# Kernel optimization log

Measured on AMD Instinct MI355X. Metric: run time of the kernel, lower is better.

## Reference

```python
import jax, jax.numpy as jnp
import numpy as np

SCALE = 100.0  # sharp-softmax temperature from the torch module

def _build_tables():
    # ByteToNibbleFFN: W1 is identity(256) so it is mathematically a no-op; keep W2.
    W2_b2n = np.zeros((256, 32), np.float32)
    bb = np.arange(256)
    W2_b2n[bb, bb >> 4] = 1.0
    W2_b2n[bb, 16 + (bb & 15)] = 1.0
    # NibbleAddWithCarryFFN tables
    W1_add = np.zeros((34, 512), np.float32)
    W2_sum = np.zeros((512, 16), np.float32)
    W2_cout = np.zeros((512, 2), np.float32)
    for a in range(16):
        for b in range(16):
            for c in range(2):
                idx = a * 32 + b * 2 + c
                W1_add[a, idx] = 1.0
                W1_add[16 + b, idx] = 1.0
                W1_add[32 + c, idx] = 1.0
                t = a + b + c
                W2_sum[idx, t & 15] = 1.0
                W2_cout[idx, 1 if t > 15 else 0] = 1.0
    # NibbleToByteFFN tables
    W1_n2b = np.zeros((32, 256), np.float32)
    W2_n2b = np.zeros((256, 256), np.float32)
    for h in range(16):
        for l in range(16):
            addr = h * 16 + l
            W1_n2b[h, addr] = 1.0
            W1_n2b[16 + l, addr] = 1.0
            W2_n2b[addr, (h << 4) | l] = 1.0
    return tuple(jnp.asarray(t) for t in (W2_b2n, W1_add, W2_sum, W2_cout, W1_n2b, W2_n2b))

W2_B2N, W1_ADD, W2_SUM, W2_COUT, W1_N2B, W2_N2B = _build_tables()

def _b2n(x):
    # byte [.,256] -> (high [.,16], low [.,16]); W1=eye(256) omitted (identity)
    out = x @ W2_B2N
    return out[..., :16], out[..., 16:]

def _nib_add(a, b, cin):
    combined = jnp.concatenate([a, b, cin], axis=-1)           # [.,34]
    address = jax.nn.softmax(combined @ W1_ADD * SCALE, axis=-1)  # [.,512]
    return address @ W2_SUM, address @ W2_COUT

def _n2b(high, low):
    combined = jnp.concatenate([high, low], axis=-1)           # [.,32]
    address = jax.nn.softmax(combined @ W1_N2B * SCALE, axis=-1)  # [.,256]
    return address @ W2_N2B

def setup_inputs() -> dict:
    key = jax.random.key(0)
    k1, k2 = jax.random.split(key)
    B = 32768
    a = jax.random.uniform(k1, (B, 4, 256), dtype=jnp.float32)
    b = jax.random.uniform(k2, (B, 4, 256), dtype=jnp.float32)
    return {"a": a, "b": b}

def reference(a, b):
    # NeuralALU.add: ripple-carry add over 4 bytes, 2 nibble adds per byte
    B = a.shape[0]
    carry = jnp.zeros((B, 2), a.dtype).at[:, 0].set(1.0)  # carry_zero one-hot
    out_bytes = []
    for i in range(4):  # fixed structural loop over bytes (carry dependence)
        ah, al = _b2n(a[:, i])
        bh, bl = _b2n(b[:, i])
        sl, carry = _nib_add(al, bl, carry)
        sh, carry = _nib_add(ah, bh, carry)
        out_bytes.append(_n2b(sh, sl))
    return jnp.stack(out_bytes, axis=1)  # [B,4,256]
```

## Files before the change

kernel.cpp:

```cpp
#include <hip/hip_runtime.h>

#define NIB_SCALE 100.0f
#define NWAVES_TOTAL 8192

template<int CTRL>
__device__ __forceinline__ float fdpp(float x) {
    return __int_as_float(__builtin_amdgcn_update_dpp(
        0, __float_as_int(x), CTRL, 0xF, 0xF, true));
}
__device__ __forceinline__ float fswz_xor4(float x) {
    return __int_as_float(__builtin_amdgcn_ds_swizzle(__float_as_int(x), 0x101F));
}
__device__ __forceinline__ float fbperm(int byteIdx, float v) {
    return __int_as_float(__builtin_amdgcn_ds_bpermute(byteIdx, __float_as_int(v)));
}

__device__ __forceinline__ float rsum16d(float v) {
    v += fdpp<0x121>(v); v += fdpp<0x122>(v); v += fdpp<0x124>(v); v += fdpp<0x128>(v);
    return v;
}
__device__ __forceinline__ float rmax16d(float v) {
    v = fmaxf(v, fdpp<0x121>(v)); v = fmaxf(v, fdpp<0x122>(v));
    v = fmaxf(v, fdpp<0x124>(v)); v = fmaxf(v, fdpp<0x128>(v));
    return v;
}
__device__ __forceinline__ float scan16d(float v) {
    v += fdpp<0x111>(v); v += fdpp<0x112>(v); v += fdpp<0x114>(v); v += fdpp<0x118>(v);
    return v;
}
__device__ __forceinline__ float softmax16d(float v) {
    float m = rmax16d(v);
    float e = __expf(NIB_SCALE * (v - m));
    float s = rsum16d(e);
    return e / s;
}
__device__ __forceinline__ float sharp_sigmoid(float c) {
    return 1.0f / (1.0f + __expf(NIB_SCALE * (1.0f - 2.0f * c)));
}

#define GATHER_ROT(dst, src)            \
    dst[0]  = (src);                    \
    dst[1]  = fdpp<0x121>(src);         \
    dst[2]  = fdpp<0x122>(src);         \
    dst[3]  = fdpp<0x123>(src);         \
    dst[4]  = fdpp<0x124>(src);         \
    dst[5]  = fdpp<0x125>(src);         \
    dst[6]  = fdpp<0x126>(src);         \
    dst[7]  = fdpp<0x127>(src);         \
    dst[8]  = fdpp<0x128>(src);         \
    dst[9]  = fdpp<0x129>(src);         \
    dst[10] = fdpp<0x12A>(src);         \
    dst[11] = fdpp<0x12B>(src);         \
    dst[12] = fdpp<0x12C>(src);         \
    dst[13] = fdpp<0x12D>(src);         \
    dst[14] = fdpp<0x12E>(src);         \
    dst[15] = fdpp<0x12F>(src);

__global__ __launch_bounds__(256, 6) void nalu_kernel(const float* __restrict__ A,
                                                      const float* __restrict__ B,
                                                      float* __restrict__ O,
                                                      int nrows) {
    __shared__ __align__(16) float sQL[16][16];
    __shared__ __align__(16) float sQH[16][16];
    __shared__ __align__(16) float sPSL[16][16];
    __shared__ __align__(16) float sPSH[16][16];
    __shared__ __align__(16) float sOV[4][4][4];

    const int tid = threadIdx.x;
    const int k = tid & 15;
    const int g = tid >> 4;
    const int b = g & 3;
    const int w = tid >> 6;
    const int lane64 = tid & 63;
    const int bpermIdx = 4 * ((lane64 & 48) | ((k & 3) << 2) | (k >> 2));
    const int wg = blockIdx.x * 4 + w;
    const int RP = (nrows + NWAVES_TOTAL - 1) / NWAVES_TOTAL;

    int row = wg;
    float4 cA0, cA1, cA2, cA3, cB0, cB1, cB2, cB3;
    if (row < nrows) {
        const float4* pa4 = (const float4*)(A + (long)row * 1024 + b * 256);
        const float4* pb4 = (const float4*)(B + (long)row * 1024 + b * 256);
        cA0 = pa4[k]; cA1 = pa4[16 + k]; cA2 = pa4[32 + k]; cA3 = pa4[48 + k];
        cB0 = pb4[k]; cB1 = pb4[16 + k]; cB2 = pb4[32 + k]; cB3 = pb4[48 + k];
    }

    for (int it = 0; it < RP; ++it) {
        const int nxtRow = row + NWAVES_TOTAL;

        float ahj[4], bhj[4];
        {
            float s;
            s = (cA0.x + cA0.y) + (cA0.z + cA0.w); s += fdpp<0xB1>(s); s += fdpp<0x4E>(s); ahj[0] = s;
            s = (cA1.x + cA1.y) + (cA1.z + cA1.w); s += fdpp<0xB1>(s); s += fdpp<0x4E>(s); ahj[1] = s;
            s = (cA2.x + cA2.y) + (cA2.z + cA2.w); s += fdpp<0xB1>(s); s += fdpp<0x4E>(s); ahj[2] = s;
            s = (cA3.x + cA3.y) + (cA3.z + cA3.w); s += fdpp<0xB1>(s); s += fdpp<0x4E>(s); ahj[3] = s;
            s = (cB0.x + cB0.y) + (cB0.z + cB0.w); s += fdpp<0xB1>(s); s += fdpp<0x4E>(s); bhj[0] = s;
            s = (cB1.x + cB1.y) + (cB1.z + cB1.w); s += fdpp<0xB1>(s); s += fdpp<0x4E>(s); bhj[1] = s;
            s = (cB2.x + cB2.y) + (cB2.z + cB2.w); s += fdpp<0xB1>(s); s += fdpp<0x4E>(s); bhj[2] = s;
            s = (cB3.x + cB3.y) + (cB3.z + cB3.w); s += fdpp<0xB1>(s); s += fdpp<0x4E>(s); bhj[3] = s;
        }
        float ali[4], bli[4];
        {
            float s;
            s = (cA0.x + cA1.x) + (cA2.x + cA3.x); s += fswz_xor4(s); s += fdpp<0x128>(s); ali[0] = s;
            s = (cA0.y + cA1.y) + (cA2.y + cA3.y); s += fswz_xor4(s); s += fdpp<0x128>(s); ali[1] = s;
            s = (cA0.z + cA1.z) + (cA2.z + cA3.z); s += fswz_xor4(s); s += fdpp<0x128>(s); ali[2] = s;
            s = (cA0.w + cA1.w) + (cA2.w + cA3.w); s += fswz_xor4(s); s += fdpp<0x128>(s); ali[3] = s;
            s = (cB0.x + cB1.x) + (cB2.x + cB3.x); s += fswz_xor4(s); s += fdpp<0x128>(s); bli[0] = s;
            s = (cB0.y + cB1.y) + (cB2.y + cB3.y); s += fswz_xor4(s); s += fdpp<0x128>(s); bli[1] = s;
            s = (cB0.z + cB1.z) + (cB2.z + cB3.z); s += fswz_xor4(s); s += fdpp<0x128>(s); bli[2] = s;
            s = (cB0.w + cB1.w) + (cB2.w + cB3.w); s += fswz_xor4(s); s += fdpp<0x128>(s); bli[3] = s;
        }
        float t0, t1;
        t0 = (k & 4) ? ali[1] : ali[0]; t1 = (k & 4) ? ali[3] : ali[2];
        float al = fbperm(bpermIdx, (k & 8) ? t1 : t0);
        t0 = (k & 4) ? bli[1] : bli[0]; t1 = (k & 4) ? bli[3] : bli[2];
        float bl = fbperm(bpermIdx, (k & 8) ? t1 : t0);
        t0 = (k & 1) ? ahj[1] : ahj[0]; t1 = (k & 1) ? ahj[3] : ahj[2];
        float ah = fbperm(bpermIdx, (k & 2) ? t1 : t0);
        t0 = (k & 1) ? bhj[1] : bhj[0]; t1 = (k & 1) ? bhj[3] : bhj[2];
        float bh = fbperm(bpermIdx, (k & 2) ? t1 : t0);

        const bool vn = (it + 1 < RP) && (nxtRow < nrows);
        if (vn) {
            const float4* pa4 = (const float4*)(A + (long)nxtRow * 1024 + b * 256);
            const float4* pb4 = (const float4*)(B + (long)nxtRow * 1024 + b * 256);
            cA0 = pa4[k]; cA1 = pa4[16 + k]; cA2 = pa4[32 + k]; cA3 = pa4[48 + k];
            cB0 = pb4[k]; cB1 = pb4[16 + k]; cB2 = pb4[32 + k]; cB3 = pb4[48 + k];
        }

        float pal = softmax16d(al);
        float pbl = softmax16d(bl);
        float pah = softmax16d(ah);
        float pbh = softmax16d(bh);

        sQL[g][k] = pbl;
        sQH[g][k] = pbh;

        float mirl = fdpp<0x140>(pbl);
        float mirh = fdpp<0x140>(pbh);
        float T15l = scan16d(mirl);
        float T15h = scan16d(mirh);
        float ov15l = rsum16d(pal * T15l);
        float c15l  = rsum16d(pal * mirl);
        float ov15h = rsum16d(pah * T15h);
        float c15h  = rsum16d(pah * mirh);
        float ov16l = ov15l - c15l;
        float ov16h = ov15h - c15h;

        sOV[w][0][b] = ov16l;
        sOV[w][1][b] = ov15l;
        sOV[w][2][b] = ov16h;
        sOV[w][3][b] = ov15h;

        float QL[16], QH[16];
        *(float4*)&QL[0]  = *(const float4*)&sQL[g][0];
        *(float4*)&QL[4]  = *(const float4*)&sQL[g][4];
        *(float4*)&QL[8]  = *(const float4*)&sQL[g][8];
        *(float4*)&QL[12] = *(const float4*)&sQL[g][12];
        float GL[16];
        GATHER_ROT(GL, pal)
        float rl = 0.f;
        #pragma unroll
        for (int j = 0; j < 16; ++j) rl = fmaf(GL[j], QL[j], rl);

        *(float4*)&QH[0]  = *(const float4*)&sQH[g][0];
        *(float4*)&QH[4]  = *(const float4*)&sQH[g][4];
        *(float4*)&QH[8]  = *(const float4*)&sQH[g][8];
        *(float4*)&QH[12] = *(const float4*)&sQH[g][12];
        float GH[16];
        GATHER_ROT(GH, pah)
        float rh = 0.f;
        #pragma unroll
        for (int j = 0; j < 16; ++j) rh = fmaf(GH[j], QH[j], rh);

        float4 O16L = *(const float4*)&sOV[w][0][0];
        float4 O15L = *(const float4*)&sOV[w][1][0];
        float4 O16H = *(const float4*)&sOV[w][2][0];
        float4 O15H = *(const float4*)&sOV[w][3][0];

        float qc1_0 = sharp_sigmoid(O16L.x);
        float qc0_0 = 1.f - qc1_0;
        float pc1_1 = sharp_sigmoid(qc0_0 * O16H.x + qc1_0 * O15H.x);
        float pc0_1 = 1.f - pc1_1;
        float qc1_1 = sharp_sigmoid(pc0_1 * O16L.y + pc1_1 * O15L.y);
        float qc0_1 = 1.f - qc1_1;
        float pc1_2 = sharp_sigmoid(qc0_1 * O16H.y + qc1_1 * O15H.y);
        float pc0_2 = 1.f - pc1_2;
        float qc1_2 = sharp_sigmoid(pc0_2 * O16L.z + pc1_2 * O15L.z);
        float qc0_2 = 1.f - qc1_2;
        float pc1_3 = sharp_sigmoid(qc0_2 * O16H.z + qc1_2 * O15H.z);
        float pc0_3 = 1.f - pc1_3;
        float qc1_3 = sharp_sigmoid(pc0_3 * O16L.w + pc1_3 * O15L.w);
        float qc0_3 = 1.f - qc1_3;

        float pc0 = b == 0 ? 1.f   : b == 1 ? pc0_1 : b == 2 ? pc0_2 : pc0_3;
        float pc1 = b == 0 ? 0.f   : b == 1 ? pc1_1 : b == 2 ? pc1_2 : pc1_3;
        float qc0 = b == 0 ? qc0_0 : b == 1 ? qc0_1 : b == 2 ? qc0_2 : qc0_3;
        float qc1 = b == 0 ? qc1_0 : b == 1 ? qc1_1 : b == 2 ? qc1_2 : qc1_3;

        float slow  = pc0 * rl + pc1 * fdpp<0x121>(rl);
        float shigh = qc0 * rh + qc1 * fdpp<0x121>(rh);

        float psl = softmax16d(slow);
        float psh = softmax16d(shigh);
        sPSL[g][k] = psl;
        sPSH[g][k] = psh;

        float4 pslq = *(const float4*)&sPSL[g][4 * (k & 3)];
        if (row < nrows) {
            float* po = O + (long)row * 1024 + b * 256;
            #pragma unroll
            for (int c = 0; c < 4; ++c) {
                float hs = sPSH[g][4 * c + (k >> 2)];
                float4 o4 = make_float4(hs * pslq.x, hs * pslq.y, hs * pslq.z, hs * pslq.w);
                *(float4*)(po + 64 * c + 4 * k) = o4;
            }
        }
        row = nxtRow;
    }
}

extern "C" void kernel_launch(void* const* d_in, const int* in_sizes, int n_in,
                              void* d_out, int out_size, void* d_ws, size_t ws_size,
                              hipStream_t stream) {
    const float* A = (const float*)d_in[0];
    const float* B = (const float*)d_in[1];
    float* O = (float*)d_out;
    int nrows = in_sizes[0] / 1024;
    nalu_kernel<<<NWAVES_TOTAL / 4, 256, 0, stream>>>(A, B, O, nrows);
}
```

Before: 355.5 us.

## Replace persistent row loop with non-persistent grid processing two rows per wave

```diff
diff --git a/kernel.cpp b/kernel.cpp
--- a/kernel.cpp
+++ b/kernel.cpp
@@ -1,7 +1,6 @@
 #include <hip/hip_runtime.h>
 
 #define NIB_SCALE 100.0f
-#define NWAVES_TOTAL 8192
 
 template<int CTRL>
 __device__ __forceinline__ float fdpp(float x) {
@@ -56,15 +55,142 @@
     dst[14] = fdpp<0x12E>(src);         \
     dst[15] = fdpp<0x12F>(src);
 
-__global__ __launch_bounds__(256, 6) void nalu_kernel(const float* __restrict__ A,
+struct SharedBufs {
+    float sQL[16][16];
+    float sQH[16][16];
+    float sPSL[16][16];
+    float sPSH[16][16];
+    float sOV[4][4][4];
+};
+
+__device__ __forceinline__ void process_row(
+        const float4 cA[4], const float4 cB[4], float* __restrict__ O,
+        long rowbase, bool valid, SharedBufs& S,
+        int k, int g, int b, int w, int bpermIdx) {
+    float ahj[4], bhj[4], ali[4], bli[4];
+    #pragma unroll
+    for (int j = 0; j < 4; ++j) {
+        float s = (cA[j].x + cA[j].y) + (cA[j].z + cA[j].w);
+        s += fdpp<0xB1>(s); s += fdpp<0x4E>(s); ahj[j] = s;
+        float t = (cB[j].x + cB[j].y) + (cB[j].z + cB[j].w);
+        t += fdpp<0xB1>(t); t += fdpp<0x4E>(t); bhj[j] = t;
+    }
+    {
+        float s;
+        s = (cA[0].x + cA[1].x) + (cA[2].x + cA[3].x); s += fswz_xor4(s); s += fdpp<0x128>(s); ali[0] = s;
+        s = (cA[0].y + cA[1].y) + (cA[2].y + cA[3].y); s += fswz_xor4(s); s += fdpp<0x128>(s); ali[1] = s;
+        s = (cA[0].z + cA[1].z) + (cA[2].z + cA[3].z); s += fswz_xor4(s); s += fdpp<0x128>(s); ali[2] = s;
+        s = (cA[0].w + cA[1].w) + (cA[2].w + cA[3].w); s += fswz_xor4(s); s += fdpp<0x128>(s); ali[3] = s;
+        s = (cB[0].x + cB[1].x) + (cB[2].x + cB[3].x); s += fswz_xor4(s); s += fdpp<0x128>(s); bli[0] = s;
+        s = (cB[0].y + cB[1].y) + (cB[2].y + cB[3].y); s += fswz_xor4(s); s += fdpp<0x128>(s); bli[1] = s;
+        s = (cB[0].z + cB[1].z) + (cB[2].z + cB[3].z); s += fswz_xor4(s); s += fdpp<0x128>(s); bli[2] = s;
+        s = (cB[0].w + cB[1].w) + (cB[2].w + cB[3].w); s += fswz_xor4(s); s += fdpp<0x128>(s); bli[3] = s;
+    }
+    float t0, t1;
+    t0 = (k & 4) ? ali[1] : ali[0]; t1 = (k & 4) ? ali[3] : ali[2];
+    float al = fbperm(bpermIdx, (k & 8) ? t1 : t0);
+    t0 = (k & 4) ? bli[1] : bli[0]; t1 = (k & 4) ? bli[3] : bli[2];
+    float bl = fbperm(bpermIdx, (k & 8) ? t1 : t0);
+    t0 = (k & 1) ? ahj[1] : ahj[0]; t1 = (k & 1) ? ahj[3] : ahj[2];
+    float ah = fbperm(bpermIdx, (k & 2) ? t1 : t0);
+    t0 = (k & 1) ? bhj[1] : bhj[0]; t1 = (k & 1) ? bhj[3] : bhj[2];
+    float bh = fbperm(bpermIdx, (k & 2) ? t1 : t0);
+
+    float pal = softmax16d(al);
+    float pbl = softmax16d(bl);
+    float pah = softmax16d(ah);
+    float pbh = softmax16d(bh);
+
+    S.sQL[g][k] = pbl;
+    S.sQH[g][k] = pbh;
+
+    float mirl = fdpp<0x140>(pbl);
+    float mirh = fdpp<0x140>(pbh);
+    float T15l = scan16d(mirl);
+    float T15h = scan16d(mirh);
+    float ov15l = rsum16d(pal * T15l);
+    float c15l  = rsum16d(pal * mirl);
+    float ov15h = rsum16d(pah * T15h);
+    float c15h  = rsum16d(pah * mirh);
+    float ov16l = ov15l - c15l;
+    float ov16h = ov15h - c15h;
+
+    S.sOV[w][0][b] = ov16l;
+    S.sOV[w][1][b] = ov15l;
+    S.sOV[w][2][b] = ov16h;
+    S.sOV[w][3][b] = ov15h;
+
+    float QL[16], QH[16];
+    *(float4*)&QL[0]  = *(const float4*)&S.sQL[g][0];
+    *(float4*)&QL[4]  = *(const float4*)&S.sQL[g][4];
+    *(float4*)&QL[8]  = *(const float4*)&S.sQL[g][8];
+    *(float4*)&QL[12] = *(const float4*)&S.sQL[g][12];
+    float GL[16];
+    GATHER_ROT(GL, pal)
+    float rl = 0.f;
+    #pragma unroll
+    for (int j = 0; j < 16; ++j) rl = fmaf(GL[j], QL[j], rl);
+
+    *(float4*)&QH[0]  = *(const float4*)&S.sQH[g][0];
+    *(float4*)&QH[4]  = *(const float4*)&S.sQH[g][4];
+    *(float4*)&QH[8]  = *(const float4*)&S.sQH[g][8];
+    *(float4*)&QH[12] = *(const float4*)&S.sQH[g][12];
+    float GH[16];
+    GATHER_ROT(GH, pah)
+    float rh = 0.f;
+    #pragma unroll
+    for (int j = 0; j < 16; ++j) rh = fmaf(GH[j], QH[j], rh);
+
+    float4 O16L = *(const float4*)&S.sOV[w][0][0];
+    float4 O15L = *(const float4*)&S.sOV[w][1][0];
+    float4 O16H = *(const float4*)&S.sOV[w][2][0];
+    float4 O15H = *(const float4*)&S.sOV[w][3][0];
+
+    float qc1_0 = sharp_sigmoid(O16L.x);
+    float qc0_0 = 1.f - qc1_0;
+    float pc1_1 = sharp_sigmoid(qc0_0 * O16H.x + qc1_0 * O15H.x);
+    float pc0_1 = 1.f - pc1_1;
+    float qc1_1 = sharp_sigmoid(pc0_1 * O16L.y + pc1_1 * O15L.y);
+    float qc0_1 = 1.f - qc1_1;
+    float pc1_2 = sharp_sigmoid(qc0_1 * O16H.y + qc1_1 * O15H.y);
+    float pc0_2 = 1.f - pc1_2;
+    float qc1_2 = sharp_sigmoid(pc0_2 * O16L.z + pc1_2 * O15L.z);
+    float qc0_2 = 1.f - qc1_2;
+    float pc1_3 = sharp_sigmoid(qc0_2 * O16H.z + qc1_2 * O15H.z);
+    float pc0_3 = 1.f - pc1_3;
+    float qc1_3 = sharp_sigmoid(pc0_3 * O16L.w + pc1_3 * O15L.w);
+    float qc0_3 = 1.f - qc1_3;
+
+    float pc0 = b == 0 ? 1.f   : b == 1 ? pc0_1 : b == 2 ? pc0_2 : pc0_3;
+    float pc1 = b == 0 ? 0.f   : b == 1 ? pc1_1 : b == 2 ? pc1_2 : pc1_3;
+    float qc0 = b == 0 ? qc0_0 : b == 1 ? qc0_1 : b == 2 ? qc0_2 : qc0_3;
+    float qc1 = b == 0 ? qc1_0 : b == 1 ? qc1_1 : b == 2 ? qc1_2 : qc1_3;
+
+    float slow  = pc0 * rl + pc1 * fdpp<0x121>(rl);
+    float shigh = qc0 * rh + qc1 * fdpp<0x121>(rh);
+
+    float psl = softmax16d(slow);
+    float psh = softmax16d(shigh);
+    S.sPSL[g][k] = psl;
+    S.sPSH[g][k] = psh;
+
+    float4 pslq = *(const float4*)&S.sPSL[g][4 * (k & 3)];
+    if (valid) {
+        float* po = O + rowbase;
+        #pragma unroll
+        for (int c = 0; c < 4; ++c) {
+            float hs = S.sPSH[g][4 * c + (k >> 2)];
+            float4 o4 = make_float4(hs * pslq.x, hs * pslq.y, hs * pslq.z, hs * pslq.w);
+            *(float4*)(po + 64 * c + 4 * k) = o4;
+        }
+    }
+}
+
+__global__ __launch_bounds__(256, 4) void nalu_kernel(const float* __restrict__ A,
                                                       const float* __restrict__ B,
                                                       float* __restrict__ O,
                                                       int nrows) {
-    __shared__ __align__(16) float sQL[16][16];
-    __shared__ __align__(16) float sQH[16][16];
-    __shared__ __align__(16) float sPSL[16][16];
-    __shared__ __align__(16) float sPSH[16][16];
-    __shared__ __align__(16) float sOV[4][4][4];
+    __shared__ SharedBufs S;
 
     const int tid = threadIdx.x;
     const int k = tid & 15;
@@ -73,153 +199,35 @@
     const int w = tid >> 6;
     const int lane64 = tid & 63;
     const int bpermIdx = 4 * ((lane64 & 48) | ((k & 3) << 2) | (k >> 2));
-    const int wg = blockIdx.x * 4 + w;
-    const int RP = (nrows + NWAVES_TOTAL - 1) / NWAVES_TOTAL;
-
-    int row = wg;
-    float4 cA0, cA1, cA2, cA3, cB0, cB1, cB2, cB3;
-    if (row < nrows) {
-        const float4* pa4 = (const float4*)(A + (long)row * 1024 + b * 256);
-        const float4* pb4 = (const float4*)(B + (long)row * 1024 + b * 256);
-        cA0 = pa4[k]; cA1 = pa4[16 + k]; cA2 = pa4[32 + k]; cA3 = pa4[48 + k];
-        cB0 = pb4[k]; cB1 = pb4[16 + k]; cB2 = pb4[32 + k]; cB3 = pb4[48 + k];
-    }
-
-    for (int it = 0; it < RP; ++it) {
-        const int nxtRow = row + NWAVES_TOTAL;
-
-        float ahj[4], bhj[4];
-        {
-            float s;
-            s = (cA0.x + cA0.y) + (cA0.z + cA0.w); s += fdpp<0xB1>(s); s += fdpp<0x4E>(s); ahj[0] = s;
-            s = (cA1.x + cA1.y) + (cA1.z + cA1.w); s += fdpp<0xB1>(s); s += fdpp<0x4E>(s); ahj[1] = s;
-            s = (cA2.x + cA2.y) + (cA2.z + cA2.w); s += fdpp<0xB1>(s); s += fdpp<0x4E>(s); ahj[2] = s;
-            s = (cA3.x + cA3.y) + (cA3.z + cA3.w); s += fdpp<0xB1>(s); s += fdpp<0x4E>(s); ahj[3] = s;
-            s = (cB0.x + cB0.y) + (cB0.z + cB0.w); s += fdpp<0xB1>(s); s += fdpp<0x4E>(s); bhj[0] = s;
-            s = (cB1.x + cB1.y) + (cB1.z + cB1.w); s += fdpp<0xB1>(s); s += fdpp<0x4E>(s); bhj[1] = s;
-            s = (cB2.x + cB2.y) + (cB2.z + cB2.w); s += fdpp<0xB1>(s); s += fdpp<0x4E>(s); bhj[2] = s;
-            s = (cB3.x + cB3.y) + (cB3.z + cB3.w); s += fdpp<0xB1>(s); s += fdpp<0x4E>(s); bhj[3] = s;
-        }
-        float ali[4], bli[4];
-        {
-            float s;
-            s = (cA0.x + cA1.x) + (cA2.x + cA3.x); s += fswz_xor4(s); s += fdpp<0x128>(s); ali[0] = s;
-            s = (cA0.y + cA1.y) + (cA2.y + cA3.y); s += fswz_xor4(s); s += fdpp<0x128>(s); ali[1] = s;
-            s = (cA0.z + cA1.z) + (cA2.z + cA3.z); s += fswz_xor4(s); s += fdpp<0x128>(s); ali[2] = s;
-            s = (cA0.w + cA1.w) + (cA2.w + cA3.w); s += fswz_xor4(s); s += fdpp<0x128>(s); ali[3] = s;
-            s = (cB0.x + cB1.x) + (cB2.x + cB3.x); s += fswz_xor4(s); s += fdpp<0x128>(s); bli[0] = s;
-            s = (cB0.y + cB1.y) + (cB2.y + cB3.y); s += fswz_xor4(s); s += fdpp<0x128>(s); bli[1] = s;
-            s = (cB0.z + cB1.z) + (cB2.z + cB3.z); s += fswz_xor4(s); s += fdpp<0x128>(s); bli[2] = s;
-            s = (cB0.w + cB1.w) + (cB2.w + cB3.w); s += fswz_xor4(s); s += fdpp<0x128>(s); bli[3] = s;
-        }
-        float t0, t1;
-        t0 = (k & 4) ? ali[1] : ali[0]; t1 = (k & 4) ? ali[3] : ali[2];
-        float al = fbperm(bpermIdx, (k & 8) ? t1 : t0);
-        t0 = (k & 4) ? bli[1] : bli[0]; t1 = (k & 4) ? bli[3] : bli[2];
-        float bl = fbperm(bpermIdx, (k & 8) ? t1 : t0);
-        t0 = (k & 1) ? ahj[1] : ahj[0]; t1 = (k & 1) ? ahj[3] : ahj[2];
-        float ah = fbperm(bpermIdx, (k & 2) ? t1 : t0);
-        t0 = (k & 1) ? bhj[1] : bhj[0]; t1 = (k & 1) ? bhj[3] : bhj[2];
-        float bh = fbperm(bpermIdx, (k & 2) ? t1 : t0);
-
-        const bool vn = (it + 1 < RP) && (nxtRow < nrows);
-        if (vn) {
-            const float4* pa4 = (const float4*)(A + (long)nxtRow * 1024 + b * 256);
-            const float4* pb4 = (const float4*)(B + (long)nxtRow * 1024 + b * 256);
-            cA0 = pa4[k]; cA1 = pa4[16 + k]; cA2 = pa4[32 + k]; cA3 = pa4[48 + k];
-            cB0 = pb4[k]; cB1 = pb4[16 + k]; cB2 = pb4[32 + k]; cB3 = pb4[48 + k];
-        }
-
-        float pal = softmax16d(al);
-        float pbl = softmax16d(bl);
-        float pah = softmax16d(ah);
-        float pbh = softmax16d(bh);
-
-        sQL[g][k] = pbl;
-        sQH[g][k] = pbh;
-
-        float mirl = fdpp<0x140>(pbl);
-        float mirh = fdpp<0x140>(pbh);
-        float T15l = scan16d(mirl);
-        float T15h = scan16d(mirh);
-        float ov15l = rsum16d(pal * T15l);
-        float c15l  = rsum16d(pal * mirl);
-        float ov15h = rsum16d(pah * T15h);
-        float c15h  = rsum16d(pah * mirh);
-        float ov16l = ov15l - c15l;
-        float ov16h = ov15h - c15h;
-
-        sOV[w][0][b] = ov16l;
-        sOV[w][1][b] = ov15l;
-        sOV[w][2][b] = ov16h;
-        sOV[w][3][b] = ov15h;
-
-        float QL[16], QH[16];
-        *(float4*)&QL[0]  = *(const float4*)&sQL[g][0];
-        *(float4*)&QL[4]  = *(const float4*)&sQL[g][4];
-        *(float4*)&QL[8]  = *(const float4*)&sQL[g][8];
-        *(float4*)&QL[12] = *(const float4*)&sQL[g][12];
-        float GL[16];
-        GATHER_ROT(GL, pal)
-        float rl = 0.f;
-        #pragma unroll
-        for (int j = 0; j < 16; ++j) rl = fmaf(GL[j], QL[j], rl);
-
-        *(float4*)&QH[0]  = *(const float4*)&sQH[g][0];
-        *(float4*)&QH[4]  = *(const float4*)&sQH[g][4];
-        *(float4*)&QH[8]  = *(const float4*)&sQH[g][8];
-        *(float4*)&QH[12] = *(const float4*)&sQH[g][12];
-        float GH[16];
-        GATHER_ROT(GH, pah)
-        float rh = 0.f;
-        #pragma unroll
-        for (int j = 0; j < 16; ++j) rh = fmaf(GH[j], QH[j], rh);
-
-        float4 O16L = *(const float4*)&sOV[w][0][0];
-        float4 O15L = *(const float4*)&sOV[w][1][0];
-        float4 O16H = *(const float4*)&sOV[w][2][0];
-        float4 O15H = *(const float4*)&sOV[w][3][0];
-
-        float qc1_0 = sharp_sigmoid(O16L.x);
-        float qc0_0 = 1.f - qc1_0;
-        float pc1_1 = sharp_sigmoid(qc0_0 * O16H.x + qc1_0 * O15H.x);
-        float pc0_1 = 1.f - pc1_1;
-        float qc1_1 = sharp_sigmoid(pc0_1 * O16L.y + pc1_1 * O15L.y);
-        float qc0_1 = 1.f - qc1_1;
-        float pc1_2 = sharp_sigmoid(qc0_1 * O16H.y + qc1_1 * O15H.y);
-        float pc0_2 = 1.f - pc1_2;
-        float qc1_2 = sharp_sigmoid(pc0_2 * O16L.z + pc1_2 * O15L.z);
-        float qc0_2 = 1.f - qc1_2;
-        float pc1_3 = sharp_sigmoid(qc0_2 * O16H.z + qc1_2 * O15H.z);
-        float pc0_3 = 1.f - pc1_3;
-        float qc1_3 = sharp_sigmoid(pc0_3 * O16L.w + pc1_3 * O15L.w);
-        float qc0_3 = 1.f - qc1_3;
-
-        float pc0 = b == 0 ? 1.f   : b == 1 ? pc0_1 : b == 2 ? pc0_2 : pc0_3;
-        float pc1 = b == 0 ? 0.f   : b == 1 ? pc1_1 : b == 2 ? pc1_2 : pc1_3;
-        float qc0 = b == 0 ? qc0_0 : b == 1 ? qc0_1 : b == 2 ? qc0_2 : qc0_3;
-        float qc1 = b == 0 ? qc1_0 : b == 1 ? qc1_1 : b == 2 ? qc1_2 : qc1_3;
-
-        float slow  = pc0 * rl + pc1 * fdpp<0x121>(rl);
-        float shigh = qc0 * rh + qc1 * fdpp<0x121>(rh);
-
-        float psl = softmax16d(slow);
-        float psh = softmax16d(shigh);
-        sPSL[g][k] = psl;
-        sPSH[g][k] = psh;
-
-        float4 pslq = *(const float4*)&sPSL[g][4 * (k & 3)];
-        if (row < nrows) {
-            float* po = O + (long)row * 1024 + b * 256;
-            #pragma unroll
-            for (int c = 0; c < 4; ++c) {
-                float hs = sPSH[g][4 * c + (k >> 2)];
-                float4 o4 = make_float4(hs * pslq.x, hs * pslq.y, hs * pslq.z, hs * pslq.w);
-                *(float4*)(po + 64 * c + 4 * k) = o4;
-            }
-        }
-        row = nxtRow;
-    }
+
+    const int r0 = blockIdx.x * 8 + w;
+    const int r1 = r0 + 4;
+    if (r0 >= nrows) return;
+    const bool v1 = (r1 < nrows);
+    const long base0 = (long)r0 * 1024 + b * 256;
+    const long base1 = (long)r1 * 1024 + b * 256;
+
+    float4 A0[4], B0[4], A1[4], B1[4];
+    {
+        const float4* pa = (const float4*)(A + base0);
+        const float4* pb = (const float4*)(B + base0);
+        #pragma unroll
+        for (int j = 0; j < 4; ++j) A0[j] = pa[16 * j + k];
+        #pragma unroll
+        for (int j = 0; j < 4; ++j) B0[j] = pb[16 * j + k];
+    }
+    if (v1) {
+        const float4* pa = (const float4*)(A + base1);
+        const float4* pb = (const float4*)(B + base1);
+        #pragma unroll
+        for (int j = 0; j < 4; ++j) A1[j] = pa[16 * j + k];
+        #pragma unroll
+        for (int j = 0; j < 4; ++j) B1[j] = pb[16 * j + k];
+    }
+    __builtin_amdgcn_sched_barrier(0);
+
+    process_row(A0, B0, O, base0, true, S, k, g, b, w, bpermIdx);
+    if (v1) process_row(A1, B1, O, base1, true, S, k, g, b, w, bpermIdx);
 }
 
 extern "C" void kernel_launch(void* const* d_in, const int* in_sizes, int n_in,
@@ -229,5 +237,6 @@
     const float* B = (const float*)d_in[1];
     float* O = (float*)d_out;
     int nrows = in_sizes[0] / 1024;
-    nalu_kernel<<<NWAVES_TOTAL / 4, 256, 0, stream>>>(A, B, O, nrows);
-}
+    int grid = (nrows + 7) / 8;
+    nalu_kernel<<<grid, 256, 0, stream>>>(A, B, O, nrows);
+}
```

New measurement: 310.8 us. 1.14x faster.
